# Kernel tuning notes

Measured on AMD Instinct MI355X. Metric: run time of the kernel, lower is better.

Reference implementation:

```python
import jax, jax.numpy as jnp
import numpy as np

THR = 1.0     # snntorch Leaky default threshold
BETA = 0.9    # args.beta
ALPHA = 2.0   # surrogate.atan default alpha

@jax.custom_vjp
def atan_spike(x):
    # Heaviside forward, arctan surrogate gradient (snntorch surrogate.atan)
    return (x > 0).astype(x.dtype)

def _aspk_fwd(x):
    return atan_spike(x), x

def _aspk_bwd(x, g):
    return (g * (ALPHA / 2.0) / (1.0 + (jnp.pi / 2.0 * ALPHA * x) ** 2),)

atan_spike.defvjp(_aspk_fwd, _aspk_bwd)

def setup_inputs() -> dict:
    key = jax.random.key(0)
    k = jax.random.split(key, 5)
    B, D, H, C = 32768, 187, 50, 5
    return {
        "x": jax.random.normal(k[0], (B, D), dtype=jnp.float32),
        "W1": jax.random.normal(k[1], (H, D), dtype=jnp.float32) * (1.0 / np.sqrt(D)),
        "b1": jax.random.normal(k[2], (H,), dtype=jnp.float32) * 0.01,
        "W2": jax.random.normal(k[3], (C, H), dtype=jnp.float32) * (1.0 / np.sqrt(H)),
        "b2": jax.random.normal(k[4], (C,), dtype=jnp.float32) * 0.01,
        "num_steps": 100,
    }

def reference(x, W1, b1, W2, b2, num_steps):
    B = x.shape[0]
    dt = x.dtype
    # fc1(x) is identical every timestep (x is static), compute once
    cur1 = x @ W1.T + b1  # [B, 50]

    def step(carry, _):
        mem1, mem2 = carry
        # Leaky: reset computed from PREVIOUS mem (detached), subtract mechanism
        reset1 = jax.lax.stop_gradient((mem1 > THR).astype(dt))
        mem1 = BETA * mem1 + cur1 - reset1 * THR
        spk1 = atan_spike(mem1 - THR)
        cur2 = spk1 @ W2.T + b2  # [B, num_classes]
        reset2 = jax.lax.stop_gradient((mem2 > THR).astype(dt))
        mem2 = BETA * mem2 + cur2 - reset2 * THR
        spk2 = atan_spike(mem2 - THR)
        return (mem1, mem2), (spk2, mem2)

    init = (jnp.zeros((B, W1.shape[0]), dt), jnp.zeros((B, W2.shape[0]), dt))
    _, (spk_rec, mem_rec) = jax.lax.scan(step, init, None, length=num_steps)
    return spk_rec, mem_rec  # each [num_steps, B, num_classes]
```

## Files before the change

kernel.cpp:

```cpp
#include <hip/hip_runtime.h>

typedef float v2f __attribute__((ext_vector_type(2)));
typedef float v4f __attribute__((ext_vector_type(4)));

#define DD   187
#define HH   50
#define PH   64
#define HPJ  14
#define HPL  16
#define NP   7
#define NC   5
#define RPB  64
#define BLK  256
#define DCH  64
#define NCHUNK 3
#define XSS  68
#define BETA 0.9f

__device__ __forceinline__ float dpp_xor1(float v) {
    return __builtin_bit_cast(float,
        __builtin_amdgcn_mov_dpp(__builtin_bit_cast(int, v), 0xB1, 0xF, 0xF, true));
}
__device__ __forceinline__ float dpp_xor2(float v) {
    return __builtin_bit_cast(float,
        __builtin_amdgcn_mov_dpp(__builtin_bit_cast(int, v), 0x4E, 0xF, 0xF, true));
}

__device__ __forceinline__ float spike1(float m) {
    float t = fmaf(m, 0x1.0p60f, -0x1.0p60f);
    return fminf(fmaxf(t, 0.f), 1.f);
}
__device__ __forceinline__ v2f spike2(v2f m) {
    const v2f BIG2  = { 0x1.0p60f,  0x1.0p60f};
    const v2f NBIG2 = {-0x1.0p60f, -0x1.0p60f};
    const v2f ONE2  = {1.f, 1.f};
    const v2f ZERO2 = {0.f, 0.f};
    v2f t = __builtin_elementwise_fma(m, BIG2, NBIG2);
    return __builtin_elementwise_min(__builtin_elementwise_max(t, ZERO2), ONE2);
}

__device__ __forceinline__ v2f vlo(v4f v) { return __builtin_shufflevector(v, v, 0, 1); }
__device__ __forceinline__ v2f vhi(v4f v) { return __builtin_shufflevector(v, v, 2, 3); }

__global__ __launch_bounds__(BLK, 2) __attribute__((amdgpu_waves_per_eu(2, 2)))
void snn_kernel(const float* __restrict__ x,
                const float* __restrict__ W1,
                const float* __restrict__ b1,
                const float* __restrict__ W2,
                const float* __restrict__ b2,
                const int*   __restrict__ nsp,
                float* __restrict__ out, int Brows)
{
    __shared__ __align__(16) float xs[RPB * XSS];
    __shared__ __align__(16) float w1t[DCH * PH];

    const int tid = threadIdx.x;
    const int p   = tid >> 2;
    const int k   = tid & 3;
    const int row = blockIdx.x * RPB + p;
    const int NS  = nsp[0];

    v2f acc[NP];
#pragma unroll
    for (int i = 0; i < NP; ++i) acc[i] = (v2f){0.f, 0.f};

    for (int ch = 0; ch < NCHUNK; ++ch) {
        const int d0 = ch * DCH;
        for (int i = tid; i < RPB * DCH; i += BLK) {
            int r = i >> 6, dd = i & 63;
            int d = d0 + dd;
            xs[r * XSS + dd] = (d < DD) ? x[(size_t)(blockIdx.x * RPB + r) * DD + d] : 0.f;
        }
        for (int i = tid; i < DCH * PH; i += BLK) {
            int dd = i >> 6, s = i & 63;
            int kk = s >> 4, j = s & 15;
            int h = kk * HPJ + j;
            int d = d0 + dd;
            w1t[dd * PH + s] = (j < HPJ && h < HH && d < DD) ? W1[h * DD + d] : 0.f;
        }
        __syncthreads();

        const float* xr = xs + p * XSS;
#pragma unroll 2
        for (int d4 = 0; d4 < DCH / 4; ++d4) {
            v4f xv4 = *(const v4f*)(xr + 4 * d4);
#pragma unroll
            for (int j = 0; j < 4; ++j) {
                int d = 4 * d4 + j;
                const float* wbase = w1t + d * PH + k * HPL;
                v4f w0 = *(const v4f*)(wbase);
                v4f w1v = *(const v4f*)(wbase + 4);
                v4f w2v = *(const v4f*)(wbase + 8);
                v2f w3 = *(const v2f*)(wbase + 12);
                float xv = xv4[j];
                v2f xvv = {xv, xv};
                acc[0] = __builtin_elementwise_fma(xvv, vlo(w0),  acc[0]);
                acc[1] = __builtin_elementwise_fma(xvv, vhi(w0),  acc[1]);
                acc[2] = __builtin_elementwise_fma(xvv, vlo(w1v), acc[2]);
                acc[3] = __builtin_elementwise_fma(xvv, vhi(w1v), acc[3]);
                acc[4] = __builtin_elementwise_fma(xvv, vlo(w2v), acc[4]);
                acc[5] = __builtin_elementwise_fma(xvv, vhi(w2v), acc[5]);
                acc[6] = __builtin_elementwise_fma(xvv, w3,       acc[6]);
            }
        }
        __syncthreads();
    }

    v2f c1[NP];
#pragma unroll
    for (int i = 0; i < NP; ++i) {
        int h0 = k * HPJ + 2 * i;
        v2f bb;
        bb.x = (h0     < HH) ? b1[h0]     : 0.f;
        bb.y = (h0 + 1 < HH) ? b1[h0 + 1] : 0.f;
        c1[i] = acc[i] + bb;
    }
    if (k == 3) c1[6].y = 2.0f;

    v2f w2r[NC][NP];
#pragma unroll
    for (int c = 0; c < NC; ++c)
#pragma unroll
        for (int i = 0; i < NP; ++i) {
            int h0 = k * HPJ + 2 * i;
            w2r[c][i].x = (h0     < HH) ? W2[c * HH + h0]     : 0.f;
            w2r[c][i].y = (h0 + 1 < HH) ? W2[c * HH + h0 + 1] : 0.f;
        }
    if (k == 3) {
#pragma unroll
        for (int c = 0; c < NC; ++c) w2r[c][6].y = b2[c];
    }

#pragma unroll
    for (int c = 0; c < NC; ++c) {
        asm volatile("" : "+v"(w2r[c][0]), "+v"(w2r[c][1]), "+v"(w2r[c][2]),
                          "+v"(w2r[c][3]), "+v"(w2r[c][4]), "+v"(w2r[c][5]),
                          "+v"(w2r[c][6]));
    }
    asm volatile("" : "+v"(c1[0]), "+v"(c1[1]), "+v"(c1[2]), "+v"(c1[3]),
                      "+v"(c1[4]), "+v"(c1[5]), "+v"(c1[6]));

    v2f m1[NP], s1[NP];
#pragma unroll
    for (int i = 0; i < NP; ++i) { m1[i] = (v2f){0.f, 0.f}; s1[i] = (v2f){0.f, 0.f}; }
    float mA = 0.f, sA = 0.f, mB = 0.f, sB = 0.f;

    const size_t stride = (size_t)Brows * NC;
    float* spkBase = out;
    float* memBase = out + (size_t)NS * stride;
    const int offA = row * NC + k;
    const int offB = row * NC + 4;
    const v2f BETA2 = {BETA, BETA};

    v2f cp[NC];
    auto S1 = [&]() {
#pragma unroll
        for (int c = 0; c < NC; ++c) cp[c] = (v2f){0.f, 0.f};
#pragma unroll
        for (int i = 0; i < NP; ++i) {
            v2f m = __builtin_elementwise_fma(BETA2, m1[i], c1[i]) - s1[i];
            m1[i] = m;
            v2f s = spike2(m);
            s1[i] = s;
#pragma unroll
            for (int c = 0; c < NC; ++c)
                cp[c] = __builtin_elementwise_fma(s, w2r[c][i], cp[c]);
        }
    };

    S1();
#pragma unroll 2
    for (int t = 0; t < NS; ++t) {
        float cur2[NC];
#pragma unroll
        for (int c = 0; c < NC; ++c) {
            float r = cp[c].x + cp[c].y;
            r += dpp_xor1(r);
            r += dpp_xor2(r);
            cur2[c] = r;
        }
        S1();

        float cA = (k == 1) ? cur2[1] : (k == 2) ? cur2[2] :
                   (k == 3) ? cur2[3] : cur2[0];
        float cB = cur2[4];

        mA = fmaf(BETA, mA, cA) - sA;
        sA = spike1(mA);
        mB = fmaf(BETA, mB, cB) - sB;
        sB = spike1(mB);

        spkBase[offA] = sA;
        memBase[offA] = mA;
        if (k == 0) { spkBase[offB] = sB; memBase[offB] = mB; }

        spkBase += stride;
        memBase += stride;
    }
}

extern "C" void kernel_launch(void* const* d_in, const int* in_sizes, int n_in,
                              void* d_out, int out_size, void* d_ws, size_t ws_size,
                              hipStream_t stream) {
    const float* x  = (const float*)d_in[0];
    const float* W1 = (const float*)d_in[1];
    const float* b1 = (const float*)d_in[2];
    const float* W2 = (const float*)d_in[3];
    const float* b2 = (const float*)d_in[4];
    const int*   ns = (const int*)d_in[5];
    int B = in_sizes[0] / DD;
    int nblocks = B / RPB;
    snn_kernel<<<nblocks, BLK, 0, stream>>>(x, W1, b1, W2, b2, ns, (float*)d_out, B);
}
```

Before: 219.9 us.

## Stage per-timestep outputs in double-buffered LDS and flush with coalesced vector stores

Each timestep's spike and membrane values are now written into shared-memory slabs that reuse the x/W1 staging buffer. After every group of four timesteps the block syncs and writes them out as contiguous float2 stores, replacing the scattered per-thread scalar global writes. Two slab sets alternate so a single barrier per tile is enough. The spike clamp also switches to fmed3, and the change adds a block barrier plus LDS traffic to the time loop.

New measurement: 226.9 us. 1.03x slower.

```diff
diff --git a/kernel.cpp b/kernel.cpp
--- a/kernel.cpp
+++ b/kernel.cpp
@@ -16,6 +16,8 @@
 #define NCHUNK 3
 #define XSS  68
 #define BETA 0.9f
+#define TILE 4
+#define SLAB 320
 
 __device__ __forceinline__ float dpp_xor1(float v) {
     return __builtin_bit_cast(float,
@@ -28,15 +30,16 @@
 
 __device__ __forceinline__ float spike1(float m) {
     float t = fmaf(m, 0x1.0p60f, -0x1.0p60f);
-    return fminf(fmaxf(t, 0.f), 1.f);
+    return __builtin_amdgcn_fmed3f(t, 0.f, 1.f);
 }
 __device__ __forceinline__ v2f spike2(v2f m) {
     const v2f BIG2  = { 0x1.0p60f,  0x1.0p60f};
     const v2f NBIG2 = {-0x1.0p60f, -0x1.0p60f};
-    const v2f ONE2  = {1.f, 1.f};
-    const v2f ZERO2 = {0.f, 0.f};
     v2f t = __builtin_elementwise_fma(m, BIG2, NBIG2);
-    return __builtin_elementwise_min(__builtin_elementwise_max(t, ZERO2), ONE2);
+    v2f s;
+    s.x = __builtin_amdgcn_fmed3f(t.x, 0.f, 1.f);
+    s.y = __builtin_amdgcn_fmed3f(t.y, 0.f, 1.f);
+    return s;
 }
 
 __device__ __forceinline__ v2f vlo(v4f v) { return __builtin_shufflevector(v, v, 0, 1); }
@@ -51,8 +54,9 @@
                 const int*   __restrict__ nsp,
                 float* __restrict__ out, int Brows)
 {
-    __shared__ __align__(16) float xs[RPB * XSS];
-    __shared__ __align__(16) float w1t[DCH * PH];
+    __shared__ __align__(16) float smem[RPB * XSS + DCH * PH];
+    float* xs  = smem;
+    float* w1t = smem + RPB * XSS;
 
     const int tid = threadIdx.x;
     const int p   = tid >> 2;
@@ -146,16 +150,18 @@
     float mA = 0.f, sA = 0.f, mB = 0.f, sB = 0.f;
 
     const size_t stride = (size_t)Brows * NC;
-    float* spkBase = out;
-    float* memBase = out + (size_t)NS * stride;
-    const int offA = row * NC + k;
-    const int offB = row * NC + 4;
+    const size_t rowBase5 = (size_t)blockIdx.x * RPB * NC;
+    float* spkT = out;
+    float* memT = out + (size_t)NS * stride;
+    const int q5  = p * NC;
+    const int q5k = q5 + k;
     const v2f BETA2 = {BETA, BETA};
+    const v2f ZERO2 = {0.f, 0.f};
 
     v2f cp[NC];
     auto S1 = [&]() {
 #pragma unroll
-        for (int c = 0; c < NC; ++c) cp[c] = (v2f){0.f, 0.f};
+        for (int c = 0; c < NC; ++c) cp[c] = ZERO2;
 #pragma unroll
         for (int i = 0; i < NP; ++i) {
             v2f m = __builtin_elementwise_fma(BETA2, m1[i], c1[i]) - s1[i];
@@ -168,9 +174,7 @@
         }
     };
 
-    S1();
-#pragma unroll 2
-    for (int t = 0; t < NS; ++t) {
+    auto STEP_T = [&](int bi, int tl) {
         float cur2[NC];
 #pragma unroll
         for (int c = 0; c < NC; ++c) {
@@ -190,12 +194,47 @@
         mB = fmaf(BETA, mB, cB) - sB;
         sB = spike1(mB);
 
-        spkBase[offA] = sA;
-        memBase[offA] = mA;
-        if (k == 0) { spkBase[offB] = sB; memBase[offB] = mB; }
-
-        spkBase += stride;
-        memBase += stride;
+        float* sb = smem + ((bi * TILE + tl) * 2 + 0) * SLAB;
+        float* mb = smem + ((bi * TILE + tl) * 2 + 1) * SLAB;
+        sb[q5k] = sA;
+        mb[q5k] = mA;
+        if (k == 0) { sb[q5 + 4] = sB; mb[q5 + 4] = mB; }
+    };
+
+    auto FLUSH = [&](int bi, int cnt, float* spkB, float* memB) {
+        const int total = cnt * SLAB;
+#pragma unroll
+        for (int u = 0; u < 2 * TILE * SLAB / (2 * BLK); ++u) {
+            int idx = u * BLK + tid;
+            if (idx < total) {
+                int slab = idx / 160;
+                int pos  = idx - slab * 160;
+                int tl2  = slab >> 1;
+                int arr  = slab & 1;
+                v2f val = *(const v2f*)(smem +
+                          (((bi * TILE + tl2) * 2 + arr) * SLAB + pos * 2));
+                float* gb = (arr ? memB : spkB) + (size_t)tl2 * stride
+                            + rowBase5 + (size_t)(pos * 2);
+                *(v2f*)gb = val;
+            }
+        }
+    };
+
+    S1();
+    int t = 0, bi = 0;
+    for (; t + TILE <= NS; t += TILE) {
+        STEP_T(bi, 0); STEP_T(bi, 1); STEP_T(bi, 2); STEP_T(bi, 3);
+        __syncthreads();
+        FLUSH(bi, TILE, spkT, memT);
+        spkT += (size_t)TILE * stride;
+        memT += (size_t)TILE * stride;
+        bi ^= 1;
+    }
+    int rem = NS - t;
+    if (rem > 0) {
+        for (int tl = 0; tl < rem; ++tl) STEP_T(bi, tl);
+        __syncthreads();
+        FLUSH(bi, rem, spkT, memT);
     }
 }
 
```

## Compute fc1 with half the threads, two rows each, redistribute via LDS

Applied to the files above, without the earlier changes.

The fc1 matmul now runs on the first 128 threads only, each handling two rows so every LDS weight load feeds two rows of FMAs. Results are written to shared memory (reusing the weight tile buffer) and read back by all 256 threads for the recurrent phase. The spike clamp is also rewritten to use the fmed3 instruction instead of a min/max pair. In exchange, half the waves sit idle during the matmul, and the extra accumulators raise register pressure and add an LDS round trip plus a barrier.

Result: slower. 231.4 us (+5.3%).

```diff
diff --git a/kernel.cpp b/kernel.cpp
--- a/kernel.cpp
+++ b/kernel.cpp
@@ -28,15 +28,16 @@
 
 __device__ __forceinline__ float spike1(float m) {
     float t = fmaf(m, 0x1.0p60f, -0x1.0p60f);
-    return fminf(fmaxf(t, 0.f), 1.f);
+    return __builtin_amdgcn_fmed3f(t, 0.f, 1.f);
 }
 __device__ __forceinline__ v2f spike2(v2f m) {
     const v2f BIG2  = { 0x1.0p60f,  0x1.0p60f};
     const v2f NBIG2 = {-0x1.0p60f, -0x1.0p60f};
-    const v2f ONE2  = {1.f, 1.f};
-    const v2f ZERO2 = {0.f, 0.f};
     v2f t = __builtin_elementwise_fma(m, BIG2, NBIG2);
-    return __builtin_elementwise_min(__builtin_elementwise_max(t, ZERO2), ONE2);
+    v2f s;
+    s.x = __builtin_amdgcn_fmed3f(t.x, 0.f, 1.f);
+    s.y = __builtin_amdgcn_fmed3f(t.y, 0.f, 1.f);
+    return s;
 }
 
 __device__ __forceinline__ v2f vlo(v4f v) { return __builtin_shufflevector(v, v, 0, 1); }
@@ -53,6 +54,7 @@
 {
     __shared__ __align__(16) float xs[RPB * XSS];
     __shared__ __align__(16) float w1t[DCH * PH];
+    float* cbuf = w1t;
 
     const int tid = threadIdx.x;
     const int p   = tid >> 2;
@@ -60,9 +62,10 @@
     const int row = blockIdx.x * RPB + p;
     const int NS  = nsp[0];
 
-    v2f acc[NP];
-#pragma unroll
-    for (int i = 0; i < NP; ++i) acc[i] = (v2f){0.f, 0.f};
+    const int pr = tid >> 2;
+    v2f acca[NP], accb[NP];
+#pragma unroll
+    for (int i = 0; i < NP; ++i) { acca[i] = (v2f){0.f, 0.f}; accb[i] = (v2f){0.f, 0.f}; }
 
     for (int ch = 0; ch < NCHUNK; ++ch) {
         const int d0 = ch * DCH;
@@ -80,31 +83,51 @@
         }
         __syncthreads();
 
-        const float* xr = xs + p * XSS;
+        if (tid < 128) {
+            const float* xr0 = xs + (2 * pr)     * XSS;
+            const float* xr1 = xs + (2 * pr + 1) * XSS;
 #pragma unroll 2
-        for (int d4 = 0; d4 < DCH / 4; ++d4) {
-            v4f xv4 = *(const v4f*)(xr + 4 * d4);
-#pragma unroll
-            for (int j = 0; j < 4; ++j) {
-                int d = 4 * d4 + j;
-                const float* wbase = w1t + d * PH + k * HPL;
-                v4f w0 = *(const v4f*)(wbase);
-                v4f w1v = *(const v4f*)(wbase + 4);
-                v4f w2v = *(const v4f*)(wbase + 8);
-                v2f w3 = *(const v2f*)(wbase + 12);
-                float xv = xv4[j];
-                v2f xvv = {xv, xv};
-                acc[0] = __builtin_elementwise_fma(xvv, vlo(w0),  acc[0]);
-                acc[1] = __builtin_elementwise_fma(xvv, vhi(w0),  acc[1]);
-                acc[2] = __builtin_elementwise_fma(xvv, vlo(w1v), acc[2]);
-                acc[3] = __builtin_elementwise_fma(xvv, vhi(w1v), acc[3]);
-                acc[4] = __builtin_elementwise_fma(xvv, vlo(w2v), acc[4]);
-                acc[5] = __builtin_elementwise_fma(xvv, vhi(w2v), acc[5]);
-                acc[6] = __builtin_elementwise_fma(xvv, w3,       acc[6]);
+            for (int d4 = 0; d4 < DCH / 4; ++d4) {
+                v4f xa4 = *(const v4f*)(xr0 + 4 * d4);
+                v4f xb4 = *(const v4f*)(xr1 + 4 * d4);
+#pragma unroll
+                for (int j = 0; j < 4; ++j) {
+                    int d = 4 * d4 + j;
+                    const float* wbase = w1t + d * PH + k * HPL;
+                    v4f w0 = *(const v4f*)(wbase);
+                    v4f w1v = *(const v4f*)(wbase + 4);
+                    v4f w2v = *(const v4f*)(wbase + 8);
+                    v2f w3 = *(const v2f*)(wbase + 12);
+                    v2f xa = {xa4[j], xa4[j]};
+                    v2f xb = {xb4[j], xb4[j]};
+                    acca[0] = __builtin_elementwise_fma(xa, vlo(w0),  acca[0]);
+                    accb[0] = __builtin_elementwise_fma(xb, vlo(w0),  accb[0]);
+                    acca[1] = __builtin_elementwise_fma(xa, vhi(w0),  acca[1]);
+                    accb[1] = __builtin_elementwise_fma(xb, vhi(w0),  accb[1]);
+                    acca[2] = __builtin_elementwise_fma(xa, vlo(w1v), acca[2]);
+                    accb[2] = __builtin_elementwise_fma(xb, vlo(w1v), accb[2]);
+                    acca[3] = __builtin_elementwise_fma(xa, vhi(w1v), acca[3]);
+                    accb[3] = __builtin_elementwise_fma(xb, vhi(w1v), accb[3]);
+                    acca[4] = __builtin_elementwise_fma(xa, vlo(w2v), acca[4]);
+                    accb[4] = __builtin_elementwise_fma(xb, vlo(w2v), accb[4]);
+                    acca[5] = __builtin_elementwise_fma(xa, vhi(w2v), acca[5]);
+                    accb[5] = __builtin_elementwise_fma(xb, vhi(w2v), accb[5]);
+                    acca[6] = __builtin_elementwise_fma(xa, w3,       acca[6]);
+                    accb[6] = __builtin_elementwise_fma(xb, w3,       accb[6]);
+                }
             }
         }
         __syncthreads();
     }
+
+    if (tid < 128) {
+#pragma unroll
+        for (int i = 0; i < NP; ++i) {
+            *(v2f*)(cbuf + (2 * pr)     * 56 + k * HPJ + 2 * i) = acca[i];
+            *(v2f*)(cbuf + (2 * pr + 1) * 56 + k * HPJ + 2 * i) = accb[i];
+        }
+    }
+    __syncthreads();
 
     v2f c1[NP];
 #pragma unroll
@@ -113,7 +136,7 @@
         v2f bb;
         bb.x = (h0     < HH) ? b1[h0]     : 0.f;
         bb.y = (h0 + 1 < HH) ? b1[h0 + 1] : 0.f;
-        c1[i] = acc[i] + bb;
+        c1[i] = *(const v2f*)(cbuf + p * 56 + k * HPJ + 2 * i) + bb;
     }
     if (k == 3) c1[6].y = 2.0f;
 
@@ -151,11 +174,12 @@
     const int offA = row * NC + k;
     const int offB = row * NC + 4;
     const v2f BETA2 = {BETA, BETA};
+    const v2f ZERO2 = {0.f, 0.f};
 
     v2f cp[NC];
     auto S1 = [&]() {
 #pragma unroll
-        for (int c = 0; c < NC; ++c) cp[c] = (v2f){0.f, 0.f};
+        for (int c = 0; c < NC; ++c) cp[c] = ZERO2;
 #pragma unroll
         for (int i = 0; i < NP; ++i) {
             v2f m = __builtin_elementwise_fma(BETA2, m1[i], c1[i]) - s1[i];
```
